# Optimization experiments

Measured on AMD Instinct MI355X. Metric: run time of the kernel, lower is better.

## Reference

```python
import jax, jax.numpy as jnp
import numpy as np

OUT_H = OUT_W = 7
SAMPLE = 2          # sample_num (sampling_ratio)
SCALE = 0.125       # spatial_scale
IMG = 1600.0        # image size implied by scale * feature size


def setup_inputs() -> dict:
    key = jax.random.key(0)
    k1, k2, k3, k4 = jax.random.split(key, 4)
    N, C, H, W = 2, 256, 200, 200
    K = 1000
    features = jax.random.normal(k1, (N, C, H, W), dtype=jnp.float32)
    b = jax.random.randint(k2, (K,), 0, N).astype(jnp.float32)
    xy = jax.random.uniform(k3, (K, 4), dtype=jnp.float32) * IMG  # raw corners
    x1 = jnp.minimum(xy[:, 0], xy[:, 2]); x2 = jnp.maximum(xy[:, 0], xy[:, 2])
    y1 = jnp.minimum(xy[:, 1], xy[:, 3]); y2 = jnp.maximum(xy[:, 1], xy[:, 3])
    rois = jnp.stack([b, x1, y1, x2, y2], axis=1)  # [K,5]
    return {"features": features, "rois": rois}


def _roi_align(features, rois):
    # Faithful port of torchvision roi_align (aligned=False, sampling_ratio=SAMPLE)
    N, C, H, W = features.shape
    K = rois.shape[0]
    b = rois[:, 0].astype(jnp.int32)
    x1 = rois[:, 1] * SCALE; y1 = rois[:, 2] * SCALE
    x2 = rois[:, 3] * SCALE; y2 = rois[:, 4] * SCALE
    roi_w = jnp.maximum(x2 - x1, 1.0)  # aligned=False forces min size 1
    roi_h = jnp.maximum(y2 - y1, 1.0)
    bin_w = roi_w / OUT_W
    bin_h = roi_h / OUT_H

    # sample coordinates: [K, out*S] along each axis
    pbin = jnp.repeat(jnp.arange(OUT_H, dtype=jnp.float32), SAMPLE)      # bin index
    sub = jnp.tile(jnp.arange(SAMPLE, dtype=jnp.float32) + 0.5, OUT_H)   # sub-sample offset
    ys = y1[:, None] + pbin[None] * bin_h[:, None] + sub[None] * bin_h[:, None] / SAMPLE  # [K,Ny]
    xs = x1[:, None] + pbin[None] * bin_w[:, None] + sub[None] * bin_w[:, None] / SAMPLE  # [K,Nx]

    def axis_terms(c, size):
        valid = (c >= -1.0) & (c <= size)        # torch: zero outside [-1, size]
        c = jnp.maximum(c, 0.0)
        lo0 = jnp.floor(c).astype(jnp.int32)
        hi_edge = lo0 >= size - 1
        lo = jnp.where(hi_edge, size - 1, lo0)
        hi = jnp.where(hi_edge, size - 1, lo0 + 1)
        c = jnp.where(hi_edge, jnp.float32(size - 1), c)
        l = c - lo.astype(jnp.float32)           # fractional part
        return valid, lo, hi, l

    vy, yl, yh, ly = axis_terms(ys, H)
    vx, xl, xh, lx = axis_terms(xs, W)
    hy, hx = 1.0 - ly, 1.0 - lx

    def gather(yi, xi):
        # [K,Ny,Nx,C] gather with per-roi batch index
        return features[b[:, None, None], :, yi[:, :, None], xi[:, None, :]]

    val = (hy[:, :, None] * hx[:, None, :])[..., None] * gather(yl, xl) \
        + (hy[:, :, None] * lx[:, None, :])[..., None] * gather(yl, xh) \
        + (ly[:, :, None] * hx[:, None, :])[..., None] * gather(yh, xl) \
        + (ly[:, :, None] * lx[:, None, :])[..., None] * gather(yh, xh)
    mask = (vy[:, :, None] & vx[:, None, :])[..., None]
    val = jnp.where(mask, val, 0.0)

    # average SAMPLE x SAMPLE points per bin -> [K,C,OUT_H,OUT_W]
    val = val.reshape(K, OUT_H, SAMPLE, OUT_W, SAMPLE, C).mean(axis=(2, 4))
    return val.transpose(0, 3, 1, 2)


def reference(features, rois):
    return _roi_align(features, rois)
```

## Files before the change

kernel.cpp:

```cpp
#include <hip/hip_runtime.h>

constexpr int C = 256, H = 200, W = 200, NB = 2;
constexpr int PH = 7, PW = 7;
constexpr int NS = 14;
constexpr float SCALE = 0.125f;
constexpr int CG = 32, NCG = C / CG;
constexpr int TS = 20;
constexpr int CGF = 8, NGROUPF = C / CGF;

typedef float f32x4 __attribute__((ext_vector_type(4)));

__global__ __launch_bounds__(256) void transpose_kernel(
    const float* __restrict__ feat, ushort* __restrict__ T)
{
    __shared__ float tile[32][36];
    int B = blockIdx.x;
    int xt = B % 7; int tmp = B / 7;
    int y  = tmp % H; tmp /= H;
    int nb = tmp & 1; int cg = tmp >> 1;
    int x0 = xt * 32;
    int xw = min(32, W - x0);

    int t = threadIdx.x;
    {
        int cl = t >> 3, xi = (t & 7) * 4;
        if (xi < xw) {
            const float* src = feat + (((size_t)nb * C + cg * CG + cl) * H + y) * W + x0 + xi;
            float4 v = *reinterpret_cast<const float4*>(src);
            tile[xi + 0][cl] = v.x; tile[xi + 1][cl] = v.y;
            tile[xi + 2][cl] = v.z; tile[xi + 3][cl] = v.w;
        }
    }
    __syncthreads();
    int xl = t >> 3, c4 = (t & 7) * 4;
    if (xl < xw) {
        float4 v = *reinterpret_cast<const float4*>(&tile[xl][c4]);
        uint u0 = __float_as_uint(v.x), u1 = __float_as_uint(v.y);
        uint u2 = __float_as_uint(v.z), u3 = __float_as_uint(v.w);
        u0 = (u0 + 0x7FFFu + ((u0 >> 16) & 1u)) >> 16;
        u1 = (u1 + 0x7FFFu + ((u1 >> 16) & 1u)) >> 16;
        u2 = (u2 + 0x7FFFu + ((u2 >> 16) & 1u)) >> 16;
        u3 = (u3 + 0x7FFFu + ((u3 >> 16) & 1u)) >> 16;
        uint2 o; o.x = u0 | (u1 << 16); o.y = u2 | (u3 << 16);
        ushort* dst = T + ((((size_t)cg * NB + nb) * H + y) * W + (x0 + xl)) * CG + c4;
        *reinterpret_cast<uint2*>(dst) = o;
    }
}

__global__ __launch_bounds__(256) void gather_kernel(
    const ushort* __restrict__ T, const float* __restrict__ rois,
    float* __restrict__ out, int K)
{
    __shared__ int   s_off[49 * TS];
    __shared__ float s_wgt[49 * TS];
    __shared__ float s_out[CG * 49];

    int B  = blockIdx.x;
    int cg = B & 7;
    int j  = B >> 3;
    int p  = j / K, k = j - p * K;

    const float* r = rois + (size_t)k * 5;
    int b = (int)r[0];
    if (b != p) return;

    float x1 = r[1]*SCALE, y1 = r[2]*SCALE, x2 = r[3]*SCALE, y2 = r[4]*SCALE;
    float bw = fmaxf(x2 - x1, 1.0f) * (1.0f / PW);
    float bh = fmaxf(y2 - y1, 1.0f) * (1.0f / PH);

    int t = threadIdx.x;
    for (int i = t; i < 49 * 16; i += 256) {
        int bin = i >> 4, cr = i & 15;
        int ph = bin / 7, pw = bin - ph * 7;
        int sy = (cr >> 3) & 1, sx = (cr >> 2) & 1, cy = (cr >> 1) & 1, cx = cr & 1;

        float ys = y1 + (float)ph * bh + ((float)sy + 0.5f) * bh * 0.5f;
        bool vy = (ys >= -1.0f) && (ys <= (float)H);
        float yc = fmaxf(ys, 0.0f);
        int ylo = (int)yc, yhi; float lyv;
        if (ylo >= H - 1) { ylo = H - 1; yhi = H - 1; lyv = 0.0f; }
        else              { yhi = ylo + 1; lyv = yc - (float)ylo; }
        int   row = cy ? yhi : ylo;
        float wy  = vy ? (cy ? lyv : 1.0f - lyv) : 0.0f;

        float xs = x1 + (float)pw * bw + ((float)sx + 0.5f) * bw * 0.5f;
        bool vx = (xs >= -1.0f) && (xs <= (float)W);
        float xc = fmaxf(xs, 0.0f);
        int xlo = (int)xc, xhi; float lxv;
        if (xlo >= W - 1) { xlo = W - 1; xhi = W - 1; lxv = 0.0f; }
        else              { xhi = xlo + 1; lxv = xc - (float)xlo; }
        int   col = cx ? xhi : xlo;
        float wx  = vx ? (cx ? lxv : 1.0f - lxv) : 0.0f;

        s_off[bin * TS + cr] = (row * W + col) * CG;
        s_wgt[bin * TS + cr] = wy * wx * 0.25f;
    }
    __syncthreads();

    if (t < 49 * 4) {
        int bin = t >> 2, q = t & 3;
        const ushort* slab = T + ((size_t)(cg * NB + p) * H * W) * CG + q * 8;
        const int*   po = s_off + bin * TS;
        const float* pg = s_wgt + bin * TS;
        int4   o0 = *reinterpret_cast<const int4*>(po + 0);
        int4   o1 = *reinterpret_cast<const int4*>(po + 4);
        int4   o2 = *reinterpret_cast<const int4*>(po + 8);
        int4   o3 = *reinterpret_cast<const int4*>(po + 12);
        float4 w0 = *reinterpret_cast<const float4*>(pg + 0);
        float4 w1 = *reinterpret_cast<const float4*>(pg + 4);
        float4 w2 = *reinterpret_cast<const float4*>(pg + 8);
        float4 w3 = *reinterpret_cast<const float4*>(pg + 12);
        uint4 d0  = *reinterpret_cast<const uint4*>(slab + o0.x);
        uint4 d1  = *reinterpret_cast<const uint4*>(slab + o0.y);
        uint4 d2  = *reinterpret_cast<const uint4*>(slab + o0.z);
        uint4 d3  = *reinterpret_cast<const uint4*>(slab + o0.w);
        uint4 d4  = *reinterpret_cast<const uint4*>(slab + o1.x);
        uint4 d5  = *reinterpret_cast<const uint4*>(slab + o1.y);
        uint4 d6  = *reinterpret_cast<const uint4*>(slab + o1.z);
        uint4 d7  = *reinterpret_cast<const uint4*>(slab + o1.w);
        uint4 d8  = *reinterpret_cast<const uint4*>(slab + o2.x);
        uint4 d9  = *reinterpret_cast<const uint4*>(slab + o2.y);
        uint4 d10 = *reinterpret_cast<const uint4*>(slab + o2.z);
        uint4 d11 = *reinterpret_cast<const uint4*>(slab + o2.w);
        uint4 d12 = *reinterpret_cast<const uint4*>(slab + o3.x);
        uint4 d13 = *reinterpret_cast<const uint4*>(slab + o3.y);
        uint4 d14 = *reinterpret_cast<const uint4*>(slab + o3.z);
        uint4 d15 = *reinterpret_cast<const uint4*>(slab + o3.w);

        float a0=0,a1=0,a2=0,a3=0,a4=0,a5=0,a6=0,a7=0;
        #define CORNER(dd, ww) \
            a0 += (ww) * __uint_as_float((dd).x << 16);          \
            a1 += (ww) * __uint_as_float((dd).x & 0xFFFF0000u);  \
            a2 += (ww) * __uint_as_float((dd).y << 16);          \
            a3 += (ww) * __uint_as_float((dd).y & 0xFFFF0000u);  \
            a4 += (ww) * __uint_as_float((dd).z << 16);          \
            a5 += (ww) * __uint_as_float((dd).z & 0xFFFF0000u);  \
            a6 += (ww) * __uint_as_float((dd).w << 16);          \
            a7 += (ww) * __uint_as_float((dd).w & 0xFFFF0000u);
        CORNER(d0,  w0.x) CORNER(d1,  w0.y) CORNER(d2,  w0.z) CORNER(d3,  w0.w)
        CORNER(d4,  w1.x) CORNER(d5,  w1.y) CORNER(d6,  w1.z) CORNER(d7,  w1.w)
        CORNER(d8,  w2.x) CORNER(d9,  w2.y) CORNER(d10, w2.z) CORNER(d11, w2.w)
        CORNER(d12, w3.x) CORNER(d13, w3.y) CORNER(d14, w3.z) CORNER(d15, w3.w)
        #undef CORNER

        float* so = s_out + (8 * q) * 49 + bin;
        so[0*49]=a0; so[1*49]=a1; so[2*49]=a2; so[3*49]=a3;
        so[4*49]=a4; so[5*49]=a5; so[6*49]=a6; so[7*49]=a7;
    }
    __syncthreads();

    float* oslab = out + ((size_t)k * C + cg * CG) * (PH * PW);
    for (int i4 = t; i4 < (CG * 49) / 4; i4 += 256) {
        f32x4 v = *reinterpret_cast<const f32x4*>(s_out + 4 * i4);
        __builtin_nontemporal_store(v, reinterpret_cast<f32x4*>(oslab + 4 * i4));
    }
}

struct __attribute__((packed, aligned(4))) f2 { float a, b; };

__global__ __launch_bounds__(256) void roi_align_fallback(
    const float* __restrict__ feat, const float* __restrict__ rois,
    float* __restrict__ out, int K)
{
    __shared__ int   s_ylo[NS], s_yhi[NS];
    __shared__ float s_wy[NS][2];
    __shared__ int   s_xb[NS];
    __shared__ float s_wx[NS][2];

    int B   = blockIdx.x;
    int xcd = B & 7;
    int j   = B >> 3;
    int p   = j / K, k = j - p * K;
    int cb  = (p * 8 + xcd) * CGF;

    const float* r = rois + (size_t)k * 5;
    int   b  = (int)r[0];
    float x1 = r[1]*SCALE, y1 = r[2]*SCALE, x2 = r[3]*SCALE, y2 = r[4]*SCALE;
    float bw = fmaxf(x2 - x1, 1.0f) * (1.0f / PW);
    float bh = fmaxf(y2 - y1, 1.0f) * (1.0f / PH);

    int t = threadIdx.x;
    if (t < NS) {
        int ph = t >> 1, s = t & 1;
        float y = y1 + (float)ph * bh + ((float)s + 0.5f) * bh * 0.5f;
        bool v = (y >= -1.0f) && (y <= (float)H);
        float yc = fmaxf(y, 0.0f);
        int lo = (int)yc, hi;
        if (lo >= H - 1) { lo = H - 1; hi = H - 1; yc = (float)(H - 1); }
        else             { hi = lo + 1; }
        float l = yc - (float)lo;
        s_ylo[t] = lo; s_yhi[t] = hi;
        s_wy[t][0] = v ? 1.0f - l : 0.0f;
        s_wy[t][1] = v ? l        : 0.0f;
    } else if (t >= 64 && t < 64 + NS) {
        int i = t - 64, pw = i >> 1, s = i & 1;
        float x = x1 + (float)pw * bw + ((float)s + 0.5f) * bw * 0.5f;
        bool v = (x >= -1.0f) && (x <= (float)W);
        float xc = fmaxf(x, 0.0f);
        int lo = (int)xc;
        if (lo >= W - 1) {
            s_xb[i] = W - 2; s_wx[i][0] = 0.0f; s_wx[i][1] = v ? 1.0f : 0.0f;
        } else {
            float l = xc - (float)lo;
            s_xb[i] = lo; s_wx[i][0] = v ? 1.0f - l : 0.0f; s_wx[i][1] = v ? l : 0.0f;
        }
    }
    __syncthreads();

    const float* img = feat + (size_t)b * (C * H * W);
    float* out_base = out + ((size_t)k * C + cb) * (PH * PW);

    for (int i = t; i < CGF * PH * PW; i += 256) {
        int cl  = i / (PH * PW);
        int bin = i - cl * (PH * PW);
        int ph  = bin / PW;
        int pw  = bin - ph * PW;
        const float* plane = img + (size_t)(cb + cl) * (H * W);

        float acc = 0.0f;
        #pragma unroll
        for (int sy = 0; sy < 2; ++sy) {
            int ysi = 2 * ph + sy;
            const float* rlo = plane + s_ylo[ysi] * W;
            const float* rhi = plane + s_yhi[ysi] * W;
            float hy = s_wy[ysi][0], ly = s_wy[ysi][1];
            #pragma unroll
            for (int sx = 0; sx < 2; ++sx) {
                int xsi = 2 * pw + sx;
                int xb = s_xb[xsi];
                float w0 = s_wx[xsi][0], w1 = s_wx[xsi][1];
                f2 vlo = *reinterpret_cast<const f2*>(rlo + xb);
                f2 vhi = *reinterpret_cast<const f2*>(rhi + xb);
                acc += hy * (w0 * vlo.a + w1 * vlo.b)
                     + ly * (w0 * vhi.a + w1 * vhi.b);
            }
        }
        __builtin_nontemporal_store(acc * 0.25f, &out_base[i]);
    }
}

extern "C" void kernel_launch(void* const* d_in, const int* in_sizes, int n_in,
                              void* d_out, int out_size, void* d_ws, size_t ws_size,
                              hipStream_t stream) {
    const float* feat = (const float*)d_in[0];
    const float* rois = (const float*)d_in[1];
    float* out = (float*)d_out;
    int K = in_sizes[1] / 5;

    size_t need = (size_t)NCG * NB * H * W * CG * sizeof(ushort);
    if (ws_size >= need) {
        ushort* T = (ushort*)d_ws;
        int tblocks = NCG * NB * H * 7;
        transpose_kernel<<<tblocks, 256, 0, stream>>>(feat, T);
        gather_kernel<<<K * NCG * NB, 256, 0, stream>>>(T, rois, out, K);
    } else {
        roi_align_fallback<<<K * NGROUPF, 256, 0, stream>>>(feat, rois, out, K);
    }
}
```

Measured before the change: 61.35 us.

## Precompute per-ROI gather offsets and weights once in the transpose kernel

Per-ROI sample offsets and bilinear weights are now computed once per ROI by extra blocks appended to the transpose kernel and stored in workspace. The gather kernel reads them from global memory instead of recomputing them in every one of its 16 blocks per ROI (8 channel groups by 2 batch slots). This removes redundant coordinate math and a shared-memory sync from the gather kernel. In exchange it adds global writes and reads of about 6 KB per ROI and needs a larger workspace.

```diff
diff --git a/kernel.cpp b/kernel.cpp
--- a/kernel.cpp
+++ b/kernel.cpp
@@ -5,54 +5,105 @@
 constexpr int NS = 14;
 constexpr float SCALE = 0.125f;
 constexpr int CG = 32, NCG = C / CG;
-constexpr int TS = 20;
+constexpr int TBLOCKS = NCG * NB * H * 7;
 constexpr int CGF = 8, NGROUPF = C / CGF;
 
 typedef float f32x4 __attribute__((ext_vector_type(4)));
 
-__global__ __launch_bounds__(256) void transpose_kernel(
-    const float* __restrict__ feat, ushort* __restrict__ T)
+__global__ __launch_bounds__(256) void prep_kernel(
+    const float* __restrict__ feat, const float* __restrict__ rois,
+    ushort* __restrict__ T, int* __restrict__ g_off, float* __restrict__ g_wgt, int K)
 {
-    __shared__ float tile[32][36];
     int B = blockIdx.x;
-    int xt = B % 7; int tmp = B / 7;
-    int y  = tmp % H; tmp /= H;
-    int nb = tmp & 1; int cg = tmp >> 1;
-    int x0 = xt * 32;
-    int xw = min(32, W - x0);
-
     int t = threadIdx.x;
-    {
-        int cl = t >> 3, xi = (t & 7) * 4;
-        if (xi < xw) {
-            const float* src = feat + (((size_t)nb * C + cg * CG + cl) * H + y) * W + x0 + xi;
-            float4 v = *reinterpret_cast<const float4*>(src);
-            tile[xi + 0][cl] = v.x; tile[xi + 1][cl] = v.y;
-            tile[xi + 2][cl] = v.z; tile[xi + 3][cl] = v.w;
-        }
+
+    if (B < TBLOCKS) {
+        __shared__ float tile[32][36];
+        int xt = B % 7; int tmp = B / 7;
+        int y  = tmp % H; tmp /= H;
+        int nb = tmp & 1; int cg = tmp >> 1;
+        int x0 = xt * 32;
+        int xw = min(32, W - x0);
+
+        {
+            int cl = t >> 3, xi = (t & 7) * 4;
+            if (xi < xw) {
+                const float* src = feat + (((size_t)nb * C + cg * CG + cl) * H + y) * W + x0 + xi;
+                float4 v = *reinterpret_cast<const float4*>(src);
+                tile[xi + 0][cl] = v.x; tile[xi + 1][cl] = v.y;
+                tile[xi + 2][cl] = v.z; tile[xi + 3][cl] = v.w;
+            }
+        }
+        __syncthreads();
+        int xl = t >> 3, c4 = (t & 7) * 4;
+        if (xl < xw) {
+            float4 v = *reinterpret_cast<const float4*>(&tile[xl][c4]);
+            uint u0 = __float_as_uint(v.x), u1 = __float_as_uint(v.y);
+            uint u2 = __float_as_uint(v.z), u3 = __float_as_uint(v.w);
+            u0 = (u0 + 0x7FFFu + ((u0 >> 16) & 1u)) >> 16;
+            u1 = (u1 + 0x7FFFu + ((u1 >> 16) & 1u)) >> 16;
+            u2 = (u2 + 0x7FFFu + ((u2 >> 16) & 1u)) >> 16;
+            u3 = (u3 + 0x7FFFu + ((u3 >> 16) & 1u)) >> 16;
+            uint2 o; o.x = u0 | (u1 << 16); o.y = u2 | (u3 << 16);
+            ushort* dst = T + ((((size_t)cg * NB + nb) * H + y) * W + (x0 + xl)) * CG + c4;
+            *reinterpret_cast<uint2*>(dst) = o;
+        }
+        return;
+    }
+
+    int k = B - TBLOCKS;
+    __shared__ int   s_ylo[NS], s_yhi[NS], s_xlo[NS], s_xhi[NS];
+    __shared__ float s_wy[NS][2], s_wx[NS][2];
+
+    const float* r = rois + (size_t)k * 5;
+    float x1 = r[1]*SCALE, y1 = r[2]*SCALE, x2 = r[3]*SCALE, y2 = r[4]*SCALE;
+    float bw = fmaxf(x2 - x1, 1.0f) * (1.0f / PW);
+    float bh = fmaxf(y2 - y1, 1.0f) * (1.0f / PH);
+
+    if (t < NS) {
+        int ph = t >> 1, s = t & 1;
+        float y = y1 + (float)ph * bh + ((float)s + 0.5f) * bh * 0.5f;
+        bool v = (y >= -1.0f) && (y <= (float)H);
+        float yc = fmaxf(y, 0.0f);
+        int lo = (int)yc, hi;
+        if (lo >= H - 1) { lo = H - 1; hi = H - 1; yc = (float)(H - 1); }
+        else             { hi = lo + 1; }
+        float l = yc - (float)lo;
+        s_ylo[t] = lo; s_yhi[t] = hi;
+        s_wy[t][0] = v ? 1.0f - l : 0.0f;
+        s_wy[t][1] = v ? l        : 0.0f;
+    } else if (t >= 64 && t < 64 + NS) {
+        int i = t - 64, pw = i >> 1, s = i & 1;
+        float x = x1 + (float)pw * bw + ((float)s + 0.5f) * bw * 0.5f;
+        bool v = (x >= -1.0f) && (x <= (float)W);
+        float xc = fmaxf(x, 0.0f);
+        int lo = (int)xc, hi;
+        if (lo >= W - 1) { lo = W - 1; hi = W - 1; xc = (float)(W - 1); }
+        else             { hi = lo + 1; }
+        float l = xc - (float)lo;
+        s_xlo[i] = lo; s_xhi[i] = hi;
+        s_wx[i][0] = v ? 1.0f - l : 0.0f;
+        s_wx[i][1] = v ? l        : 0.0f;
     }
     __syncthreads();
-    int xl = t >> 3, c4 = (t & 7) * 4;
-    if (xl < xw) {
-        float4 v = *reinterpret_cast<const float4*>(&tile[xl][c4]);
-        uint u0 = __float_as_uint(v.x), u1 = __float_as_uint(v.y);
-        uint u2 = __float_as_uint(v.z), u3 = __float_as_uint(v.w);
-        u0 = (u0 + 0x7FFFu + ((u0 >> 16) & 1u)) >> 16;
-        u1 = (u1 + 0x7FFFu + ((u1 >> 16) & 1u)) >> 16;
-        u2 = (u2 + 0x7FFFu + ((u2 >> 16) & 1u)) >> 16;
-        u3 = (u3 + 0x7FFFu + ((u3 >> 16) & 1u)) >> 16;
-        uint2 o; o.x = u0 | (u1 << 16); o.y = u2 | (u3 << 16);
-        ushort* dst = T + ((((size_t)cg * NB + nb) * H + y) * W + (x0 + xl)) * CG + c4;
-        *reinterpret_cast<uint2*>(dst) = o;
+
+    for (int e = t; e < 49 * 16; e += 256) {
+        int bin = e >> 4, cr = e & 15;
+        int ph = bin / 7, pw = bin - ph * 7;
+        int sy = (cr >> 3) & 1, sx = (cr >> 2) & 1, cy = (cr >> 1) & 1, cx = cr & 1;
+        int ysi = 2 * ph + sy, xsi = 2 * pw + sx;
+        int row = cy ? s_yhi[ysi] : s_ylo[ysi];
+        int col = cx ? s_xhi[xsi] : s_xlo[xsi];
+        g_off[(size_t)k * 784 + e] = (row * W + col) * CG;
+        g_wgt[(size_t)k * 784 + e] = s_wy[ysi][cy] * s_wx[xsi][cx] * 0.25f;
     }
 }
 
 __global__ __launch_bounds__(256) void gather_kernel(
     const ushort* __restrict__ T, const float* __restrict__ rois,
+    const int* __restrict__ g_off, const float* __restrict__ g_wgt,
     float* __restrict__ out, int K)
 {
-    __shared__ int   s_off[49 * TS];
-    __shared__ float s_wgt[49 * TS];
     __shared__ float s_out[CG * 49];
 
     int B  = blockIdx.x;
@@ -64,44 +115,11 @@
     int b = (int)r[0];
     if (b != p) return;
 
-    float x1 = r[1]*SCALE, y1 = r[2]*SCALE, x2 = r[3]*SCALE, y2 = r[4]*SCALE;
-    float bw = fmaxf(x2 - x1, 1.0f) * (1.0f / PW);
-    float bh = fmaxf(y2 - y1, 1.0f) * (1.0f / PH);
-
     int t = threadIdx.x;
-    for (int i = t; i < 49 * 16; i += 256) {
-        int bin = i >> 4, cr = i & 15;
-        int ph = bin / 7, pw = bin - ph * 7;
-        int sy = (cr >> 3) & 1, sx = (cr >> 2) & 1, cy = (cr >> 1) & 1, cx = cr & 1;
-
-        float ys = y1 + (float)ph * bh + ((float)sy + 0.5f) * bh * 0.5f;
-        bool vy = (ys >= -1.0f) && (ys <= (float)H);
-        float yc = fmaxf(ys, 0.0f);
-        int ylo = (int)yc, yhi; float lyv;
-        if (ylo >= H - 1) { ylo = H - 1; yhi = H - 1; lyv = 0.0f; }
-        else              { yhi = ylo + 1; lyv = yc - (float)ylo; }
-        int   row = cy ? yhi : ylo;
-        float wy  = vy ? (cy ? lyv : 1.0f - lyv) : 0.0f;
-
-        float xs = x1 + (float)pw * bw + ((float)sx + 0.5f) * bw * 0.5f;
-        bool vx = (xs >= -1.0f) && (xs <= (float)W);
-        float xc = fmaxf(xs, 0.0f);
-        int xlo = (int)xc, xhi; float lxv;
-        if (xlo >= W - 1) { xlo = W - 1; xhi = W - 1; lxv = 0.0f; }
-        else              { xhi = xlo + 1; lxv = xc - (float)xlo; }
-        int   col = cx ? xhi : xlo;
-        float wx  = vx ? (cx ? lxv : 1.0f - lxv) : 0.0f;
-
-        s_off[bin * TS + cr] = (row * W + col) * CG;
-        s_wgt[bin * TS + cr] = wy * wx * 0.25f;
-    }
-    __syncthreads();
-
     if (t < 49 * 4) {
         int bin = t >> 2, q = t & 3;
-        const ushort* slab = T + ((size_t)(cg * NB + p) * H * W) * CG + q * 8;
-        const int*   po = s_off + bin * TS;
-        const float* pg = s_wgt + bin * TS;
+        const int*   po = g_off + (size_t)k * 784 + bin * 16;
+        const float* pg = g_wgt + (size_t)k * 784 + bin * 16;
         int4   o0 = *reinterpret_cast<const int4*>(po + 0);
         int4   o1 = *reinterpret_cast<const int4*>(po + 4);
         int4   o2 = *reinterpret_cast<const int4*>(po + 8);
@@ -110,6 +128,8 @@
         float4 w1 = *reinterpret_cast<const float4*>(pg + 4);
         float4 w2 = *reinterpret_cast<const float4*>(pg + 8);
         float4 w3 = *reinterpret_cast<const float4*>(pg + 12);
+
+        const ushort* slab = T + ((size_t)(cg * NB + p) * H * W) * CG + q * 8;
         uint4 d0  = *reinterpret_cast<const uint4*>(slab + o0.x);
         uint4 d1  = *reinterpret_cast<const uint4*>(slab + o0.y);
         uint4 d2  = *reinterpret_cast<const uint4*>(slab + o0.z);
@@ -247,12 +267,14 @@
     float* out = (float*)d_out;
     int K = in_sizes[1] / 5;
 
-    size_t need = (size_t)NCG * NB * H * W * CG * sizeof(ushort);
+    size_t t_bytes = (size_t)NCG * NB * H * W * CG * sizeof(ushort);
+    size_t need = t_bytes + (size_t)K * 784 * (sizeof(int) + sizeof(float));
     if (ws_size >= need) {
-        ushort* T = (ushort*)d_ws;
-        int tblocks = NCG * NB * H * 7;
-        transpose_kernel<<<tblocks, 256, 0, stream>>>(feat, T);
-        gather_kernel<<<K * NCG * NB, 256, 0, stream>>>(T, rois, out, K);
+        ushort* T    = (ushort*)d_ws;
+        int*   g_off = (int*)((char*)d_ws + t_bytes);
+        float* g_wgt = (float*)((char*)d_ws + t_bytes + (size_t)K * 784 * sizeof(int));
+        prep_kernel<<<TBLOCKS + K, 256, 0, stream>>>(feat, rois, T, g_off, g_wgt, K);
+        gather_kernel<<<K * NCG * NB, 256, 0, stream>>>(T, rois, g_off, g_wgt, out, K);
     } else {
         roi_align_fallback<<<K * NGROUPF, 256, 0, stream>>>(feat, rois, out, K);
     }
```

After: 69.83 us. 1.14x slower.
